# Performance work log

Measured on AMD Instinct MI355X. Metric: run time of the kernel, lower is better.

The kernel has to match this reference:

```python
import jax, jax.numpy as jnp
import numpy as np

L, D, H, FF = 6, 1024, 16, 4096
HD = D // H
EPS = 1e-5


def _ln(x, g, b):
    m = jnp.mean(x, axis=-1, keepdims=True)
    v = jnp.var(x, axis=-1, keepdims=True)
    return (x - m) * jax.lax.rsqrt(v + EPS) * g + b


def _heads(t, S, B):  # [S,B,D] -> [B*H,S,HD]
    return t.reshape(S, B * H, HD).swapaxes(0, 1)


def _attn(q, k, v, mask):
    # q,k,v: [B*H, Sq/Sk, HD]; q pre-scaled
    scores = jnp.einsum('bqd,bkd->bqk', q, k)
    if mask is not None:
        scores = scores + mask  # broadcast [1,Sq,Sk]
    p = jax.nn.softmax(scores, axis=-1)
    return jnp.einsum('bqk,bkd->bqd', p, v)


def _self_attn(x, w_qkv, b_qkv, w_out, b_out, mask):
    S, B, _ = x.shape
    qkv = x @ w_qkv.T + b_qkv  # [S,B,3D]
    q, k, v = jnp.split(qkv, 3, axis=-1)
    q = q * (HD ** -0.5)
    a = _attn(_heads(q, S, B), _heads(k, S, B), _heads(v, S, B), mask)
    a = a.swapaxes(0, 1).reshape(S, B, D)
    return a @ w_out.T + b_out


def _cross_attn(x, mem, w_q, b_q, w_kv, b_kv, w_out, b_out):
    S, B, _ = x.shape
    Sm = mem.shape[0]
    q = (x @ w_q.T + b_q) * (HD ** -0.5)
    kv = mem @ w_kv.T + b_kv  # [Sm,B,2D]
    k, v = jnp.split(kv, 2, axis=-1)
    a = _attn(_heads(q, S, B), _heads(k, Sm, B), _heads(v, Sm, B), None)
    a = a.swapaxes(0, 1).reshape(S, B, D)
    return a @ w_out.T + b_out


def _ffn(x, w1, b1, w2, b2):
    h = jax.nn.gelu(x @ w1.T + b1, approximate=False)
    return h @ w2.T + b2


def setup_inputs() -> dict:
    key = jax.random.key(0)
    ks = iter(jax.random.split(key, 64))
    def p(*shape, s=0.02):
        return (jax.random.normal(next(ks), shape, dtype=jnp.float32) * s)
    inp = {
        'src': jax.random.normal(next(ks), (512, 8, D), dtype=jnp.float32),
        'tgt': jax.random.normal(next(ks), (512, 8, D), dtype=jnp.float32),
        # encoder params (stacked over L layers)
        'enc_qkv_w': p(L, 3 * D, D), 'enc_qkv_b': p(L, 3 * D),
        'enc_out_w': p(L, D, D), 'enc_out_b': p(L, D),
        'enc_ln1_g': jnp.ones((L, D)), 'enc_ln1_b': jnp.zeros((L, D)),
        'enc_fc1_w': p(L, FF, D), 'enc_fc1_b': p(L, FF),
        'enc_fc2_w': p(L, D, FF), 'enc_fc2_b': p(L, D),
        'enc_ln2_g': jnp.ones((L, D)), 'enc_ln2_b': jnp.zeros((L, D)),
        'enc_norm_g': jnp.ones((D,)), 'enc_norm_b': jnp.zeros((D,)),
        # decoder params
        'dec_qkv_w': p(L, 3 * D, D), 'dec_qkv_b': p(L, 3 * D),
        'dec_sout_w': p(L, D, D), 'dec_sout_b': p(L, D),
        'dec_ln1_g': jnp.ones((L, D)), 'dec_ln1_b': jnp.zeros((L, D)),
        'dec_q_w': p(L, D, D), 'dec_q_b': p(L, D),
        'dec_kv_w': p(L, 2 * D, D), 'dec_kv_b': p(L, 2 * D),
        'dec_cout_w': p(L, D, D), 'dec_cout_b': p(L, D),
        'dec_ln2_g': jnp.ones((L, D)), 'dec_ln2_b': jnp.zeros((L, D)),
        'dec_fc1_w': p(L, FF, D), 'dec_fc1_b': p(L, FF),
        'dec_fc2_w': p(L, D, FF), 'dec_fc2_b': p(L, D),
        'dec_ln3_g': jnp.ones((L, D)), 'dec_ln3_b': jnp.zeros((L, D)),
        'dec_norm_g': jnp.ones((D,)), 'dec_norm_b': jnp.zeros((D,)),
    }
    return inp


def reference(src, tgt,
              enc_qkv_w, enc_qkv_b, enc_out_w, enc_out_b,
              enc_ln1_g, enc_ln1_b, enc_fc1_w, enc_fc1_b,
              enc_fc2_w, enc_fc2_b, enc_ln2_g, enc_ln2_b,
              enc_norm_g, enc_norm_b,
              dec_qkv_w, dec_qkv_b, dec_sout_w, dec_sout_b,
              dec_ln1_g, dec_ln1_b, dec_q_w, dec_q_b,
              dec_kv_w, dec_kv_b, dec_cout_w, dec_cout_b,
              dec_ln2_g, dec_ln2_b, dec_fc1_w, dec_fc1_b,
              dec_fc2_w, dec_fc2_b, dec_ln3_g, dec_ln3_b,
              dec_norm_g, dec_norm_b):
    St = tgt.shape[0]
    # causal additive mask [1,St,St]
    causal = jnp.where(jnp.tril(jnp.ones((St, St), dtype=bool)), 0.0, -jnp.inf)
    causal = causal[None].astype(src.dtype)

    # ---- encoder ----
    x = src
    for i in range(L):
        x = x + _self_attn(_ln(x, enc_ln1_g[i], enc_ln1_b[i]),
                           enc_qkv_w[i], enc_qkv_b[i], enc_out_w[i], enc_out_b[i], None)
        x = x + _ffn(_ln(x, enc_ln2_g[i], enc_ln2_b[i]),
                     enc_fc1_w[i], enc_fc1_b[i], enc_fc2_w[i], enc_fc2_b[i])
    memory = _ln(x, enc_norm_g, enc_norm_b)

    # ---- decoder ----
    y = tgt
    for i in range(L):
        y = y + _self_attn(_ln(y, dec_ln1_g[i], dec_ln1_b[i]),
                           dec_qkv_w[i], dec_qkv_b[i], dec_sout_w[i], dec_sout_b[i], causal)
        y = y + _cross_attn(_ln(y, dec_ln2_g[i], dec_ln2_b[i]), memory,
                            dec_q_w[i], dec_q_b[i], dec_kv_w[i], dec_kv_b[i],
                            dec_cout_w[i], dec_cout_b[i])
        y = y + _ffn(_ln(y, dec_ln3_g[i], dec_ln3_b[i]),
                     dec_fc1_w[i], dec_fc1_b[i], dec_fc2_w[i], dec_fc2_b[i])
    return _ln(y, dec_norm_g, dec_norm_b)
```

## Files before the change

kernel.cpp:

```cpp
#include <hip/hip_runtime.h>

typedef __attribute__((ext_vector_type(4))) float f32x4;
typedef __attribute__((ext_vector_type(8))) short short8;
typedef unsigned int u32;
typedef unsigned short u16;
typedef __attribute__((ext_vector_type(2))) u32 u32x2;
typedef __attribute__((ext_vector_type(4))) u32 u32x4;

#define DEV __device__ __forceinline__
#define GBAR __builtin_amdgcn_s_barrier()
#define SB0  __builtin_amdgcn_sched_barrier(0)

DEV u16 f2b(float f){
  u32 u = __builtin_bit_cast(u32, f);
  u32 r = u + 0x7fffu + ((u >> 16) & 1u);
  return (u16)(r >> 16);
}
DEV u32 pk2(float a, float b){ return (u32)f2b(a) | ((u32)f2b(b) << 16); }

DEV void gload16(const void* g, void* l){
  __builtin_amdgcn_global_load_lds((const __attribute__((address_space(1))) void*)g,
                                   (__attribute__((address_space(3))) void*)l, 16, 0, 0);
}
DEV u32 lds_addr(void* p){
  return (u32)(unsigned long long)(__attribute__((address_space(3))) char*)p;
}

__global__ __launch_bounds__(256) void cvt_k(const float* __restrict__ in,
                                             u16* __restrict__ out, int n8)
{
  int i = blockIdx.x*256 + threadIdx.x;
  const int stride = gridDim.x*256;
  for (; i < n8; i += stride){
    const float4 a = ((const float4*)in)[2*i];
    const float4 b = ((const float4*)in)[2*i+1];
    u32x4 r;
    r.x = pk2(a.x,a.y); r.y = pk2(a.z,a.w);
    r.z = pk2(b.x,b.y); r.w = pk2(b.z,b.w);
    ((u32x4*)out)[i] = r;
  }
}

template<int OUT_F32>
__global__ __launch_bounds__(256) void ln_k(const float* __restrict__ x,
    const float* __restrict__ gam, const float* __restrict__ bet,
    void* __restrict__ out)
{
  const int row = blockIdx.x, tid = threadIdx.x;
  const float4 v = ((const float4*)(x + row*1024))[tid];
  float s = (v.x + v.y) + (v.z + v.w);
  float q = (v.x*v.x + v.y*v.y) + (v.z*v.z + v.w*v.w);
  #pragma unroll
  for (int m = 1; m < 64; m <<= 1){ s += __shfl_xor(s, m); q += __shfl_xor(q, m); }
  __shared__ float ps[4], pq[4];
  if ((tid & 63) == 0){ ps[tid>>6] = s; pq[tid>>6] = q; }
  __syncthreads();
  s = (ps[0]+ps[1]) + (ps[2]+ps[3]);
  q = (pq[0]+pq[1]) + (pq[2]+pq[3]);
  const float mean = s * (1.f/1024.f);
  const float var  = q * (1.f/1024.f) - mean*mean;
  const float rstd = rsqrtf(var + 1e-5f);
  const float4 gg = ((const float4*)gam)[tid];
  const float4 bb = ((const float4*)bet)[tid];
  const float o0 = (v.x-mean)*rstd*gg.x + bb.x;
  const float o1 = (v.y-mean)*rstd*gg.y + bb.y;
  const float o2 = (v.z-mean)*rstd*gg.z + bb.z;
  const float o3 = (v.w-mean)*rstd*gg.w + bb.w;
  if (OUT_F32){
    float4 r; r.x=o0; r.y=o1; r.z=o2; r.w=o3;
    ((float4*)out)[row*256 + tid] = r;
  } else {
    u32x2 r; r.x = pk2(o0,o1); r.y = pk2(o2,o3);
    ((u32x2*)out)[row*256 + tid] = r;
  }
}

template<int DO_GELU, int DO_RES, int OUT_F32>
__global__ __launch_bounds__(256,2) void gemm_k(
    const u16* __restrict__ A, const u16* __restrict__ W,
    const float* __restrict__ bias, const float* __restrict__ res,
    void* __restrict__ Cout, int M, int N, int K)
{
  __shared__ char sA[16384];
  __shared__ char sB[16384];
  const int tid = threadIdx.x;
  const int lane = tid & 63, w = tid >> 6;
  const int wr = w >> 1, wc = w & 1;
  const int g = lane >> 4, c16 = lane & 15;

  const u32 nwg = gridDim.x * gridDim.y;
  u32 flat = blockIdx.x + gridDim.x * blockIdx.y;
  {
    const u32 q = nwg >> 3, r = nwg & 7;
    const u32 xcd = flat & 7, idx = flat >> 3;
    flat = (xcd < r ? xcd*(q+1) : r*(q+1) + (xcd-r)*q) + idx;
  }
  const int m0 = (int)(flat % gridDim.x) * 128;
  const int n0 = (int)(flat / gridDim.x) * 128;

  f32x4 acc[4][4];
  #pragma unroll
  for (int m = 0; m < 4; m++)
    #pragma unroll
    for (int n = 0; n < 4; n++) acc[m][n] = (f32x4){0.f,0.f,0.f,0.f};

  const int arow = tid >> 3, achk = tid & 7;
  const int acg = achk ^ (arow & 7);
  const u16* aSrc = A + (size_t)(m0 + arow)*K + acg*8;
  const u16* wSrc = W + (size_t)(n0 + arow)*K + acg*8;
  char* aDst = sA + w*1024;
  char* bDst = sB + w*1024;

  for (int kk = 0; kk < K; kk += 64){
    __syncthreads();
    #pragma unroll
    for (int i = 0; i < 4; i++){
      gload16(aSrc + (size_t)i*32*K + kk, aDst + i*4096);
      gload16(wSrc + (size_t)i*32*K + kk, bDst + i*4096);
    }
    __syncthreads();
    #pragma unroll
    for (int ks = 0; ks < 2; ks++){
      short8 af[4], bf[4];
      #pragma unroll
      for (int m = 0; m < 4; m++){
        const int row = wr*64 + m*16 + c16;
        af[m] = *(const short8*)(sA + row*128 + (((ks*4 + g) ^ (row & 7)) << 4));
      }
      #pragma unroll
      for (int n = 0; n < 4; n++){
        const int row = wc*64 + n*16 + c16;
        bf[n] = *(const short8*)(sB + row*128 + (((ks*4 + g) ^ (row & 7)) << 4));
      }
      #pragma unroll
      for (int m = 0; m < 4; m++)
        #pragma unroll
        for (int n = 0; n < 4; n++)
          acc[m][n] = __builtin_amdgcn_mfma_f32_16x16x32_bf16(af[m], bf[n], acc[m][n], 0,0,0);
    }
  }
  #pragma unroll
  for (int n = 0; n < 4; n++){
    const int col = n0 + wc*64 + n*16 + c16;
    const float bv = bias[col];
    #pragma unroll
    for (int m = 0; m < 4; m++){
      const int rbase = m0 + wr*64 + m*16 + g*4;
      #pragma unroll
      for (int r = 0; r < 4; r++){
        float v = acc[m][n][r] + bv;
        if (DO_GELU) v = 0.5f*v*(1.f + erff(v*0.70710678118654752f));
        if (DO_RES)  v += res[(size_t)(rbase + r)*N + col];
        if (OUT_F32) ((float*)Cout)[(size_t)(rbase + r)*N + col] = v;
        else         ((u16*)Cout)[(size_t)(rbase + r)*N + col] = f2b(v);
      }
    }
  }
}

template<int DO_GELU, int DO_RES, int OUT_F32>
__global__ __launch_bounds__(256,2) void gemm64_k(
    const u16* __restrict__ A, const u16* __restrict__ W,
    const float* __restrict__ bias, const float* __restrict__ res,
    void* __restrict__ Cout, int M, int N, int K)
{
  __shared__ char sA[8192];
  __shared__ char sB[8192];
  const int tid = threadIdx.x;
  const int lane = tid & 63, w = tid >> 6;
  const int wr = w >> 1, wc = w & 1;
  const int g = lane >> 4, c16 = lane & 15;

  const u32 nwg = gridDim.x * gridDim.y;
  u32 flat = blockIdx.x + gridDim.x * blockIdx.y;
  {
    const u32 q = nwg >> 3, r = nwg & 7;
    const u32 xcd = flat & 7, idx = flat >> 3;
    flat = (xcd < r ? xcd*(q+1) : r*(q+1) + (xcd-r)*q) + idx;
  }
  const int m0 = (int)(flat % gridDim.x) * 64;
  const int n0 = (int)(flat / gridDim.x) * 64;

  f32x4 acc[2][2];
  #pragma unroll
  for (int m = 0; m < 2; m++)
    #pragma unroll
    for (int n = 0; n < 2; n++) acc[m][n] = (f32x4){0.f,0.f,0.f,0.f};

  const int arow = tid >> 3, achk = tid & 7;
  const int acg = achk ^ (arow & 7);
  const u16* aSrc = A + (size_t)(m0 + arow)*K + acg*8;
  const u16* wSrc = W + (size_t)(n0 + arow)*K + acg*8;
  char* aDst = sA + w*1024;
  char* bDst = sB + w*1024;

  for (int kk = 0; kk < K; kk += 64){
    __syncthreads();
    #pragma unroll
    for (int i = 0; i < 2; i++){
      gload16(aSrc + (size_t)i*32*K + kk, aDst + i*4096);
      gload16(wSrc + (size_t)i*32*K + kk, bDst + i*4096);
    }
    __syncthreads();
    #pragma unroll
    for (int ks = 0; ks < 2; ks++){
      short8 af[2], bf[2];
      #pragma unroll
      for (int m = 0; m < 2; m++){
        const int row = wr*32 + m*16 + c16;
        af[m] = *(const short8*)(sA + row*128 + (((ks*4 + g) ^ (row & 7)) << 4));
      }
      #pragma unroll
      for (int n = 0; n < 2; n++){
        const int row = wc*32 + n*16 + c16;
        bf[n] = *(const short8*)(sB + row*128 + (((ks*4 + g) ^ (row & 7)) << 4));
      }
      #pragma unroll
      for (int m = 0; m < 2; m++)
        #pragma unroll
        for (int n = 0; n < 2; n++)
          acc[m][n] = __builtin_amdgcn_mfma_f32_16x16x32_bf16(af[m], bf[n], acc[m][n], 0,0,0);
    }
  }
  #pragma unroll
  for (int n = 0; n < 2; n++){
    const int col = n0 + wc*32 + n*16 + c16;
    const float bv = bias[col];
    #pragma unroll
    for (int m = 0; m < 2; m++){
      const int rbase = m0 + wr*32 + m*16 + g*4;
      #pragma unroll
      for (int r = 0; r < 4; r++){
        float v = acc[m][n][r] + bv;
        if (DO_GELU) v = 0.5f*v*(1.f + erff(v*0.70710678118654752f));
        if (DO_RES)  v += res[(size_t)(rbase + r)*N + col];
        if (OUT_F32) ((float*)Cout)[(size_t)(rbase + r)*N + col] = v;
        else         ((u16*)Cout)[(size_t)(rbase + r)*N + col] = f2b(v);
      }
    }
  }
}

template<int CAUSAL>
__global__ __launch_bounds__(256,2) void attn_k(
    const u16* __restrict__ Qb, int qB, int qS,
    const u16* __restrict__ Kb, int kB, int kS,
    const u16* __restrict__ Vb, int vB, int vS,
    u16* __restrict__ Ob, int oB, int oS, float scale)
{
  __shared__ char smem[16384];
  const int tid = threadIdx.x;
  const int lane = tid & 63, w = tid >> 6;
  const int g = lane >> 4, c16 = lane & 15;
  const int qt = blockIdx.x, bh = blockIdx.y;
  const int b = bh >> 4, h = bh & 15;
  const u16* Q  = Qb + b*qB + h*64;
  const u16* Kp = Kb + b*kB + h*64;
  const u16* Vp = Vb + b*vB + h*64;
  u16*       Op = Ob + b*oB + h*64;

  const int qrow = qt*64 + w*16 + c16;
  const short8 bq0 = *(const short8*)(Q + qrow*qS + g*8);
  const short8 bq1 = *(const short8*)(Q + qrow*qS + 32 + g*8);

  f32x4 o[4];
  #pragma unroll
  for (int d = 0; d < 4; d++) o[d] = (f32x4){0.f,0.f,0.f,0.f};
  float mrun = -__builtin_inff(), lrun = 0.f;

  const int srow = tid >> 3, schk = tid & 7;
  const u16* kSrc = Kp + srow*kS + (schk ^ (srow & 7))*8;
  const u16* vSrc = Vp + srow*vS + schk*8;
  const u32 vtr0 = lds_addr(smem) + 8192 + (8*g + (c16 >> 2))*128 + (c16 & 3)*8;

  auto STAGE = [&](int p, int j0){
    gload16(kSrc + (size_t)j0*kS, smem + p*4096 + w*1024);
    gload16(vSrc + (size_t)j0*vS, smem + 8192 + p*4096 + w*1024);
  };
  auto COMPUTE = [&](int p, int j0){
    char* Ks = smem + p*4096;
    f32x4 st[2];
    #pragma unroll
    for (int t = 0; t < 2; t++){
      const int row = t*16 + c16;
      const int rx = row & 7;
      const short8 ka0 = *(const short8*)(Ks + row*128 + ((g ^ rx) << 4));
      const short8 ka1 = *(const short8*)(Ks + row*128 + (((4 + g) ^ rx) << 4));
      f32x4 z = (f32x4){0.f,0.f,0.f,0.f};
      z = __builtin_amdgcn_mfma_f32_16x16x32_bf16(ka0, bq0, z, 0,0,0);
      z = __builtin_amdgcn_mfma_f32_16x16x32_bf16(ka1, bq1, z, 0,0,0);
      st[t] = z;
    }
    float mloc = -__builtin_inff();
    #pragma unroll
    for (int t = 0; t < 2; t++)
      #pragma unroll
      for (int r = 0; r < 4; r++){
        float sv = st[t][r]*scale;
        if (CAUSAL){ if (j0 + t*16 + g*4 + r > qrow) sv = -__builtin_inff(); }
        st[t][r] = sv;
        mloc = fmaxf(mloc, sv);
      }
    mloc = fmaxf(mloc, __shfl_xor(mloc, 16));
    mloc = fmaxf(mloc, __shfl_xor(mloc, 32));
    const float mnew = fmaxf(mrun, mloc);
    const float corr = __expf(mrun - mnew);
    float psum = 0.f;
    u32 pk00, pk01, pk10, pk11;
    {
      float p0 = __expf(st[0][0]-mnew), p1 = __expf(st[0][1]-mnew);
      float p2 = __expf(st[0][2]-mnew), p3 = __expf(st[0][3]-mnew);
      psum += (p0+p1) + (p2+p3);
      pk00 = pk2(p0,p1); pk01 = pk2(p2,p3);
      p0 = __expf(st[1][0]-mnew); p1 = __expf(st[1][1]-mnew);
      p2 = __expf(st[1][2]-mnew); p3 = __expf(st[1][3]-mnew);
      psum += (p0+p1) + (p2+p3);
      pk10 = pk2(p0,p1); pk11 = pk2(p2,p3);
    }
    psum += __shfl_xor(psum, 16);
    psum += __shfl_xor(psum, 32);
    lrun = lrun*corr + psum;
    mrun = mnew;
    #pragma unroll
    for (int d = 0; d < 4; d++){
      o[d][0]*=corr; o[d][1]*=corr; o[d][2]*=corr; o[d][3]*=corr;
    }
    const int sl0 = c16 | (((g << 1)     & 3) << 4);
    const int sl1 = c16 | ((((g << 1)+1) & 3) << 4);
    const u32 a00 = (u32)__shfl((int)pk00, sl0), a01 = (u32)__shfl((int)pk01, sl0);
    const u32 a02 = (u32)__shfl((int)pk00, sl1), a03 = (u32)__shfl((int)pk01, sl1);
    const u32 a10 = (u32)__shfl((int)pk10, sl0), a11 = (u32)__shfl((int)pk11, sl0);
    const u32 a12 = (u32)__shfl((int)pk10, sl1), a13 = (u32)__shfl((int)pk11, sl1);
    const bool hi = g >= 2;
    union { short8 s; u32 u[4]; } pb;
    pb.u[0] = hi ? a10 : a00;
    pb.u[1] = hi ? a11 : a01;
    pb.u[2] = hi ? a12 : a02;
    pb.u[3] = hi ? a13 : a03;

    const u32 vtr = vtr0 + p*4096;
    u32x2 t00,t01,t10,t11,t20,t21,t30,t31;
    asm volatile("ds_read_b64_tr_b16 %0, %1 offset:0"   : "=v"(t00) : "v"(vtr));
    asm volatile("ds_read_b64_tr_b16 %0, %1 offset:512" : "=v"(t01) : "v"(vtr));
    asm volatile("ds_read_b64_tr_b16 %0, %1 offset:32"  : "=v"(t10) : "v"(vtr));
    asm volatile("ds_read_b64_tr_b16 %0, %1 offset:544" : "=v"(t11) : "v"(vtr));
    asm volatile("ds_read_b64_tr_b16 %0, %1 offset:64"  : "=v"(t20) : "v"(vtr));
    asm volatile("ds_read_b64_tr_b16 %0, %1 offset:576" : "=v"(t21) : "v"(vtr));
    asm volatile("ds_read_b64_tr_b16 %0, %1 offset:96"  : "=v"(t30) : "v"(vtr));
    asm volatile("ds_read_b64_tr_b16 %0, %1 offset:608" : "=v"(t31) : "v"(vtr));
    asm volatile("s_waitcnt lgkmcnt(0)" ::: "memory");
    __builtin_amdgcn_sched_barrier(0);
    union { short8 s; u32x2 d[2]; } v0u, v1u, v2u, v3u;
    v0u.d[0]=t00; v0u.d[1]=t01;
    v1u.d[0]=t10; v1u.d[1]=t11;
    v2u.d[0]=t20; v2u.d[1]=t21;
    v3u.d[0]=t30; v3u.d[1]=t31;
    o[0] = __builtin_amdgcn_mfma_f32_16x16x32_bf16(v0u.s, pb.s, o[0], 0,0,0);
    o[1] = __builtin_amdgcn_mfma_f32_16x16x32_bf16(v1u.s, pb.s, o[1], 0,0,0);
    o[2] = __builtin_amdgcn_mfma_f32_16x16x32_bf16(v2u.s, pb.s, o[2], 0,0,0);
    o[3] = __builtin_amdgcn_mfma_f32_16x16x32_bf16(v3u.s, pb.s, o[3], 0,0,0);
  };

  const int nCh = CAUSAL ? (2*qt + 2) : 16;
  STAGE(0, 0);
  for (int jc = 0; jc < nCh - 1; ++jc){
    STAGE((jc+1) & 1, (jc+1)*32);
    asm volatile("s_waitcnt vmcnt(2)" ::: "memory");
    GBAR; SB0;
    COMPUTE(jc & 1, jc*32);
    SB0; GBAR;
  }
  asm volatile("s_waitcnt vmcnt(0)" ::: "memory");
  GBAR; SB0;
  COMPUTE((nCh-1) & 1, (nCh-1)*32);
  SB0; GBAR;

  const float inv = 1.f / lrun;
  char* Olds = smem;
  #pragma unroll
  for (int dd = 0; dd < 4; dd++){
    u32x2 val;
    val.x = pk2(o[dd][0]*inv, o[dd][1]*inv);
    val.y = pk2(o[dd][2]*inv, o[dd][3]*inv);
    const int row = w*16 + c16;
    const int off = 32*dd + 8*g;
    const int chunk = off >> 4, rem = off & 15;
    *(u32x2*)(Olds + row*128 + ((chunk ^ (row & 7)) << 4) + rem) = val;
  }
  __syncthreads();
  const int orow = tid >> 2, oc = tid & 3;
  #pragma unroll
  for (int i = 0; i < 2; i++){
    const int ch = oc*2 + i;
    const u32x4 vv = *(const u32x4*)(Olds + orow*128 + ((ch ^ (orow & 7)) << 4));
    *(u32x4*)(Op + (qt*64 + orow)*oS + ch*8) = vv;
  }
}

static inline int cvt_grid(int n8){ int g = (n8 + 255) / 256; return g > 2048 ? 2048 : g; }

extern "C" void kernel_launch(void* const* d_in, const int* in_sizes, int n_in,
                              void* d_out, int out_size, void* d_ws, size_t ws_size,
                              hipStream_t stream)
{
  (void)in_sizes; (void)n_in; (void)out_size; (void)ws_size;
  const float* src      = (const float*)d_in[0];
  const float* tgt      = (const float*)d_in[1];
  const float* e_qkv_w  = (const float*)d_in[2];
  const float* e_qkv_b  = (const float*)d_in[3];
  const float* e_out_w  = (const float*)d_in[4];
  const float* e_out_b  = (const float*)d_in[5];
  const float* e_ln1_g  = (const float*)d_in[6];
  const float* e_ln1_b  = (const float*)d_in[7];
  const float* e_fc1_w  = (const float*)d_in[8];
  const float* e_fc1_b  = (const float*)d_in[9];
  const float* e_fc2_w  = (const float*)d_in[10];
  const float* e_fc2_b  = (const float*)d_in[11];
  const float* e_ln2_g  = (const float*)d_in[12];
  const float* e_ln2_b  = (const float*)d_in[13];
  const float* e_nrm_g  = (const float*)d_in[14];
  const float* e_nrm_b  = (const float*)d_in[15];
  const float* dc_qkv_w = (const float*)d_in[16];
  const float* dc_qkv_b = (const float*)d_in[17];
  const float* dc_sout_w= (const float*)d_in[18];
  const float* dc_sout_b= (const float*)d_in[19];
  const float* dc_ln1_g = (const float*)d_in[20];
  const float* dc_ln1_b = (const float*)d_in[21];
  const float* dc_q_w   = (const float*)d_in[22];
  const float* dc_q_b   = (const float*)d_in[23];
  const float* dc_kv_w  = (const float*)d_in[24];
  const float* dc_kv_b  = (const float*)d_in[25];
  const float* dc_cout_w= (const float*)d_in[26];
  const float* dc_cout_b= (const float*)d_in[27];
  const float* dc_ln2_g = (const float*)d_in[28];
  const float* dc_ln2_b = (const float*)d_in[29];
  const float* dc_fc1_w = (const float*)d_in[30];
  const float* dc_fc1_b = (const float*)d_in[31];
  const float* dc_fc2_w = (const float*)d_in[32];
  const float* dc_fc2_b = (const float*)d_in[33];
  const float* dc_ln3_g = (const float*)d_in[34];
  const float* dc_ln3_b = (const float*)d_in[35];
  const float* dc_nrm_g = (const float*)d_in[36];
  const float* dc_nrm_b = (const float*)d_in[37];

  char* ws = (char*)d_ws;
  u16*  ln_out = (u16*)(ws);
  u16*  attn_o = (u16*)(ws + (8u<<20));
  u16*  membuf = (u16*)(ws + (16u<<20));
  float* xres  = (float*)(ws + (24u<<20));
  u16*  region = (u16*)(ws + (40u<<20));
  u16*  qkv   = region;
  u16*  hbuf  = region;
  u16*  qbuf  = region;
  u16*  kvbuf = region + (4u<<20);

  const dim3 blk(256);
  const int M = 4096;

  u16* wb = (u16*)(ws + (72u<<20));
  size_t woff = 0;
  auto CV = [&](const float* wsrc, size_t n)->u16* {
    u16* p = wb + woff; woff += n;
    cvt_k<<<cvt_grid((int)(n >> 3)), blk, 0, stream>>>(wsrc, p, (int)(n >> 3));
    return p;
  };
  u16* Weqkv = CV(e_qkv_w,  6ull*3072*1024);
  u16* Weout = CV(e_out_w,  6ull*1024*1024);
  u16* Wefc1 = CV(e_fc1_w,  6ull*4096*1024);
  u16* Wefc2 = CV(e_fc2_w,  6ull*4096*1024);
  u16* Wdqkv = CV(dc_qkv_w, 6ull*3072*1024);
  u16* Wdsout= CV(dc_sout_w,6ull*1024*1024);
  u16* Wdq   = CV(dc_q_w,   6ull*1024*1024);
  u16* Wdkv  = CV(dc_kv_w,  6ull*2048*1024);
  u16* Wdcout= CV(dc_cout_w,6ull*1024*1024);
  u16* Wdfc1 = CV(dc_fc1_w, 6ull*4096*1024);
  u16* Wdfc2 = CV(dc_fc2_w, 6ull*4096*1024);

  for (int i = 0; i < 6; i++){
    const float* xin = i ? xres : src;
    ln_k<0><<<4096, blk, 0, stream>>>(xin, e_ln1_g + i*1024, e_ln1_b + i*1024, ln_out);
    gemm_k<0,0,0><<<dim3(32, 24), blk, 0, stream>>>(ln_out,
        Weqkv + (size_t)i*3145728, e_qkv_b + i*3072, nullptr, qkv, M, 3072, 1024);
    attn_k<0><<<dim3(8,128), blk, 0, stream>>>(qkv, 3072, 24576,
        qkv+1024, 3072, 24576, qkv+2048, 3072, 24576, attn_o, 1024, 8192, 0.125f);
    gemm64_k<0,1,1><<<dim3(64, 16), blk, 0, stream>>>(attn_o,
        Weout + (size_t)i*1048576, e_out_b + i*1024, xin, xres, M, 1024, 1024);
    ln_k<0><<<4096, blk, 0, stream>>>(xres, e_ln2_g + i*1024, e_ln2_b + i*1024, ln_out);
    gemm_k<1,0,0><<<dim3(32, 32), blk, 0, stream>>>(ln_out,
        Wefc1 + (size_t)i*4194304, e_fc1_b + i*4096, nullptr, hbuf, M, 4096, 1024);
    gemm64_k<0,1,1><<<dim3(64, 16), blk, 0, stream>>>(hbuf,
        Wefc2 + (size_t)i*4194304, e_fc2_b + i*1024, xres, xres, M, 1024, 4096);
  }
  ln_k<0><<<4096, blk, 0, stream>>>(xres, e_nrm_g, e_nrm_b, membuf);

  for (int i = 0; i < 6; i++){
    const float* yin = i ? xres : tgt;
    ln_k<0><<<4096, blk, 0, stream>>>(yin, dc_ln1_g + i*1024, dc_ln1_b + i*1024, ln_out);
    gemm_k<0,0,0><<<dim3(32, 24), blk, 0, stream>>>(ln_out,
        Wdqkv + (size_t)i*3145728, dc_qkv_b + i*3072, nullptr, qkv, M, 3072, 1024);
    attn_k<1><<<dim3(8,128), blk, 0, stream>>>(qkv, 3072, 24576,
        qkv+1024, 3072, 24576, qkv+2048, 3072, 24576, attn_o, 1024, 8192, 0.125f);
    gemm64_k<0,1,1><<<dim3(64, 16), blk, 0, stream>>>(attn_o,
        Wdsout + (size_t)i*1048576, dc_sout_b + i*1024, yin, xres, M, 1024, 1024);
    ln_k<0><<<4096, blk, 0, stream>>>(xres, dc_ln2_g + i*1024, dc_ln2_b + i*1024, ln_out);
    gemm64_k<0,0,0><<<dim3(64, 16), blk, 0, stream>>>(ln_out,
        Wdq + (size_t)i*1048576, dc_q_b + i*1024, nullptr, qbuf, M, 1024, 1024);
    gemm64_k<0,0,0><<<dim3(64, 32), blk, 0, stream>>>(membuf,
        Wdkv + (size_t)i*2097152, dc_kv_b + i*2048, nullptr, kvbuf, M, 2048, 1024);
    attn_k<0><<<dim3(8,128), blk, 0, stream>>>(qbuf, 1024, 8192,
        kvbuf, 2048, 16384, kvbuf+1024, 2048, 16384, attn_o, 1024, 8192, 0.125f);
    gemm64_k<0,1,1><<<dim3(64, 16), blk, 0, stream>>>(attn_o,
        Wdcout + (size_t)i*1048576, dc_cout_b + i*1024, xres, xres, M, 1024, 1024);
    ln_k<0><<<4096, blk, 0, stream>>>(xres, dc_ln3_g + i*1024, dc_ln3_b + i*1024, ln_out);
    gemm_k<1,0,0><<<dim3(32, 32), blk, 0, stream>>>(ln_out,
        Wdfc1 + (size_t)i*4194304, dc_fc1_b + i*4096, nullptr, hbuf, M, 4096, 1024);
    gemm64_k<0,1,1><<<dim3(64, 16), blk, 0, stream>>>(hbuf,
        Wdfc2 + (size_t)i*4194304, dc_fc2_b + i*1024, xres, xres, M, 1024, 4096);
  }
  ln_k<1><<<4096, blk, 0, stream>>>(xres, dc_nrm_g, dc_nrm_b, d_out);
}
```

Baseline: 3.719 ms.

## Add 256x256-tile 8-wave GEMM for QKV and FC1 projections

Adds a new 512-thread GEMM kernel with 256x256 output tiles, 128KB double-buffered LDS and interleaved global-to-LDS staging across four MFMA phases per K step. It replaces the older 128-tile gemm_k for the QKV and FC1 (with GELU) projections, to raise operand reuse and cut global/LDS traffic per FLOP. The grids shrink to 192 and 256 workgroups, which can leave CUs idle or underfilled on a 256-CU device. The epilogue writes bf16 with scalar strided stores. The barrier macro also switches from the builtin to inline-asm s_barrier with a memory clobber.

```diff
diff --git a/kernel.cpp b/kernel.cpp
--- a/kernel.cpp
+++ b/kernel.cpp
@@ -8,8 +8,8 @@
 typedef __attribute__((ext_vector_type(4))) u32 u32x4;
 
 #define DEV __device__ __forceinline__
-#define GBAR __builtin_amdgcn_s_barrier()
 #define SB0  __builtin_amdgcn_sched_barrier(0)
+#define HBAR asm volatile("s_barrier" ::: "memory")
 
 DEV u16 f2b(float f){
   u32 u = __builtin_bit_cast(u32, f);
@@ -72,6 +72,151 @@
   } else {
     u32x2 r; r.x = pk2(o0,o1); r.y = pk2(o2,o3);
     ((u32x2*)out)[row*256 + tid] = r;
+  }
+}
+
+template<int DO_GELU>
+__global__ __launch_bounds__(512,2) void gemm256_k(
+    const u16* __restrict__ A, const u16* __restrict__ W,
+    const float* __restrict__ bias, u16* __restrict__ Cout,
+    int M, int N, int K)
+{
+  __shared__ char lds[131072];
+  const int tid = threadIdx.x;
+  const int lane = tid & 63, wid = tid >> 6;
+  const int wr = wid >> 2, wc = wid & 3;
+  const int g = lane >> 4, c16 = lane & 15;
+
+  const u32 nwg = gridDim.x * gridDim.y;
+  u32 flat = blockIdx.x + gridDim.x * blockIdx.y;
+  {
+    const u32 q = nwg >> 3, r = nwg & 7;
+    const u32 xcd = flat & 7, idx = flat >> 3;
+    flat = (xcd < r ? xcd*(q+1) : r*(q+1) + (xcd-r)*q) + idx;
+  }
+  const int m0 = (int)(flat % gridDim.x) * 256;
+  const int n0 = (int)(flat / gridDim.x) * 256;
+
+  f32x4 acc[8][4];
+  #pragma unroll
+  for (int m = 0; m < 8; m++)
+    #pragma unroll
+    for (int n = 0; n < 4; n++) acc[m][n] = (f32x4){0.f,0.f,0.f,0.f};
+
+  const int srow = tid >> 3, schk = tid & 7;
+  const int scg = schk ^ (srow & 7);
+  const u16* aS = A + (size_t)(m0 + srow)*K + scg*8;
+  const u16* wS = W + (size_t)(n0 + srow)*K + scg*8;
+
+  auto SG = [&](const u16* base, int regionOff, int sb, int half, int i, int kk){
+    gload16(base + (size_t)(half*128 + i*64)*K + kk,
+            lds + sb*65536 + regionOff + half*16384 + i*8192 + tid*16);
+  };
+  short8 af[4][2], bf[4][2];
+  auto LDA4 = [&](char* bufA, int mbase){
+    #pragma unroll
+    for (int i = 0; i < 4; i++){
+      const int r = (mbase + i)*16 + c16;
+      const int rx = r & 7;
+      af[i][0] = *(const short8*)(bufA + r*128 + ((g ^ rx) << 4));
+      af[i][1] = *(const short8*)(bufA + r*128 + (((4 + g) ^ rx) << 4));
+    }
+  };
+  auto LDB2 = [&](char* bufB, int nbase){
+    #pragma unroll
+    for (int i = 0; i < 2; i++){
+      const int r = (wc & 1)*64 + (nbase + i)*16 + c16;
+      const int rx = r & 7;
+      bf[nbase+i][0] = *(const short8*)(bufB + r*128 + ((g ^ rx) << 4));
+      bf[nbase+i][1] = *(const short8*)(bufB + r*128 + (((4 + g) ^ rx) << 4));
+    }
+  };
+
+  const int NT = K >> 6;
+  SG(wS, 32768, 0, 0, 0, 0); SG(wS, 32768, 0, 0, 1, 0);
+  SG(wS, 32768, 0, 1, 0, 0); SG(wS, 32768, 0, 1, 1, 0);
+  SG(aS, 0,     0, 0, 0, 0); SG(aS, 0,     0, 0, 1, 0);
+  SG(aS, 0,     0, 1, 0, 0); SG(aS, 0,     0, 1, 1, 0);
+  asm volatile("s_waitcnt vmcnt(1)" ::: "memory");
+  HBAR;
+
+  for (int t = 0; t < NT; ++t){
+    const int b = t & 1, sb = b ^ 1;
+    const int skk = (t+1) << 6;
+    const bool st = (t+1 < NT);
+    char* bufA = lds + b*65536 + wr*16384;
+    char* bufB = lds + b*65536 + 32768 + (wc >> 1)*16384;
+
+    LDA4(bufA, 0); LDB2(bufB, 0);
+    if (st){ SG(wS, 32768, sb, 0, 0, skk); SG(wS, 32768, sb, 0, 1, skk); }
+    HBAR;
+    asm volatile("s_waitcnt lgkmcnt(0)" ::: "memory"); SB0;
+    __builtin_amdgcn_s_setprio(1);
+    #pragma unroll
+    for (int ks = 0; ks < 2; ks++)
+      #pragma unroll
+      for (int i = 0; i < 4; i++)
+        #pragma unroll
+        for (int j = 0; j < 2; j++)
+          acc[i][j] = __builtin_amdgcn_mfma_f32_16x16x32_bf16(af[i][ks], bf[j][ks], acc[i][j], 0,0,0);
+    __builtin_amdgcn_s_setprio(0);
+    LDB2(bufB, 2);
+    if (st){ SG(wS, 32768, sb, 1, 0, skk); SG(wS, 32768, sb, 1, 1, skk); }
+    HBAR;
+    asm volatile("s_waitcnt lgkmcnt(0)" ::: "memory"); SB0;
+    __builtin_amdgcn_s_setprio(1);
+    #pragma unroll
+    for (int ks = 0; ks < 2; ks++)
+      #pragma unroll
+      for (int i = 0; i < 4; i++)
+        #pragma unroll
+        for (int j = 2; j < 4; j++)
+          acc[i][j] = __builtin_amdgcn_mfma_f32_16x16x32_bf16(af[i][ks], bf[j][ks], acc[i][j], 0,0,0);
+    __builtin_amdgcn_s_setprio(0);
+    if (st) asm volatile("s_waitcnt vmcnt(4)" ::: "memory");
+    else    asm volatile("s_waitcnt vmcnt(0)" ::: "memory");
+    HBAR;
+    LDA4(bufA, 4);
+    if (st){ SG(aS, 0, sb, 0, 0, skk); SG(aS, 0, sb, 0, 1, skk); }
+    asm volatile("s_waitcnt lgkmcnt(0)" ::: "memory"); SB0;
+    __builtin_amdgcn_s_setprio(1);
+    #pragma unroll
+    for (int ks = 0; ks < 2; ks++)
+      #pragma unroll
+      for (int i = 0; i < 4; i++)
+        #pragma unroll
+        for (int j = 0; j < 2; j++)
+          acc[4+i][j] = __builtin_amdgcn_mfma_f32_16x16x32_bf16(af[i][ks], bf[j][ks], acc[4+i][j], 0,0,0);
+    __builtin_amdgcn_s_setprio(0);
+    if (st){ SG(aS, 0, sb, 1, 0, skk); SG(aS, 0, sb, 1, 1, skk); }
+    HBAR;
+    __builtin_amdgcn_s_setprio(1);
+    #pragma unroll
+    for (int ks = 0; ks < 2; ks++)
+      #pragma unroll
+      for (int i = 0; i < 4; i++)
+        #pragma unroll
+        for (int j = 2; j < 4; j++)
+          acc[4+i][j] = __builtin_amdgcn_mfma_f32_16x16x32_bf16(af[i][ks], bf[j][ks], acc[4+i][j], 0,0,0);
+    __builtin_amdgcn_s_setprio(0);
+    if (st) asm volatile("s_waitcnt vmcnt(1)" ::: "memory");
+    HBAR;
+  }
+
+  #pragma unroll
+  for (int n = 0; n < 4; n++){
+    const int col = n0 + wc*64 + n*16 + c16;
+    const float bv = bias[col];
+    #pragma unroll
+    for (int m = 0; m < 8; m++){
+      const int rbase = m0 + wr*128 + m*16 + g*4;
+      #pragma unroll
+      for (int r = 0; r < 4; r++){
+        float v = acc[m][n][r] + bv;
+        if (DO_GELU) v = 0.5f*v*(1.f + erff(v*0.70710678118654752f));
+        Cout[(size_t)(rbase + r)*N + col] = f2b(v);
+      }
+    }
   }
 }
 
@@ -366,14 +511,14 @@
   for (int jc = 0; jc < nCh - 1; ++jc){
     STAGE((jc+1) & 1, (jc+1)*32);
     asm volatile("s_waitcnt vmcnt(2)" ::: "memory");
-    GBAR; SB0;
+    HBAR; SB0;
     COMPUTE(jc & 1, jc*32);
-    SB0; GBAR;
+    SB0; HBAR;
   }
   asm volatile("s_waitcnt vmcnt(0)" ::: "memory");
-  GBAR; SB0;
+  HBAR; SB0;
   COMPUTE((nCh-1) & 1, (nCh-1)*32);
-  SB0; GBAR;
+  SB0; HBAR;
 
   const float inv = 1.f / lrun;
   char* Olds = smem;
@@ -455,6 +600,7 @@
   u16*  kvbuf = region + (4u<<20);
 
   const dim3 blk(256);
+  const dim3 blk512(512);
   const int M = 4096;
 
   u16* wb = (u16*)(ws + (72u<<20));
@@ -479,15 +625,15 @@
   for (int i = 0; i < 6; i++){
     const float* xin = i ? xres : src;
     ln_k<0><<<4096, blk, 0, stream>>>(xin, e_ln1_g + i*1024, e_ln1_b + i*1024, ln_out);
-    gemm_k<0,0,0><<<dim3(32, 24), blk, 0, stream>>>(ln_out,
-        Weqkv + (size_t)i*3145728, e_qkv_b + i*3072, nullptr, qkv, M, 3072, 1024);
+    gemm256_k<0><<<dim3(16, 12), blk512, 0, stream>>>(ln_out,
+        Weqkv + (size_t)i*3145728, e_qkv_b + i*3072, qkv, M, 3072, 1024);
     attn_k<0><<<dim3(8,128), blk, 0, stream>>>(qkv, 3072, 24576,
         qkv+1024, 3072, 24576, qkv+2048, 3072, 24576, attn_o, 1024, 8192, 0.125f);
     gemm64_k<0,1,1><<<dim3(64, 16), blk, 0, stream>>>(attn_o,
         Weout + (size_t)i*1048576, e_out_b + i*1024, xin, xres, M, 1024, 1024);
     ln_k<0><<<4096, blk, 0, stream>>>(xres, e_ln2_g + i*1024, e_ln2_b + i*1024, ln_out);
-    gemm_k<1,0,0><<<dim3(32, 32), blk, 0, stream>>>(ln_out,
-        Wefc1 + (size_t)i*4194304, e_fc1_b + i*4096, nullptr, hbuf, M, 4096, 1024);
+    gemm256_k<1><<<dim3(16, 16), blk512, 0, stream>>>(ln_out,
+        Wefc1 + (size_t)i*4194304, e_fc1_b + i*4096, hbuf, M, 4096, 1024);
     gemm64_k<0,1,1><<<dim3(64, 16), blk, 0, stream>>>(hbuf,
         Wefc2 + (size_t)i*4194304, e_fc2_b + i*1024, xres, xres, M, 1024, 4096);
   }
@@ -496,8 +642,8 @@
   for (int i = 0; i < 6; i++){
     const float* yin = i ? xres : tgt;
     ln_k<0><<<4096, blk, 0, stream>>>(yin, dc_ln1_g + i*1024, dc_ln1_b + i*1024, ln_out);
-    gemm_k<0,0,0><<<dim3(32, 24), blk, 0, stream>>>(ln_out,
-        Wdqkv + (size_t)i*3145728, dc_qkv_b + i*3072, nullptr, qkv, M, 3072, 1024);
+    gemm256_k<0><<<dim3(16, 12), blk512, 0, stream>>>(ln_out,
+        Wdqkv + (size_t)i*3145728, dc_qkv_b + i*3072, qkv, M, 3072, 1024);
     attn_k<1><<<dim3(8,128), blk, 0, stream>>>(qkv, 3072, 24576,
         qkv+1024, 3072, 24576, qkv+2048, 3072, 24576, attn_o, 1024, 8192, 0.125f);
     gemm64_k<0,1,1><<<dim3(64, 16), blk, 0, stream>>>(attn_o,
@@ -512,8 +658,8 @@
     gemm64_k<0,1,1><<<dim3(64, 16), blk, 0, stream>>>(attn_o,
         Wdcout + (size_t)i*1048576, dc_cout_b + i*1024, xres, xres, M, 1024, 1024);
     ln_k<0><<<4096, blk, 0, stream>>>(xres, dc_ln3_g + i*1024, dc_ln3_b + i*1024, ln_out);
-    gemm_k<1,0,0><<<dim3(32, 32), blk, 0, stream>>>(ln_out,
-        Wdfc1 + (size_t)i*4194304, dc_fc1_b + i*4096, nullptr, hbuf, M, 4096, 1024);
+    gemm256_k<1><<<dim3(16, 16), blk512, 0, stream>>>(ln_out,
+        Wdfc1 + (size_t)i*4194304, dc_fc1_b + i*4096, hbuf, M, 4096, 1024);
     gemm64_k<0,1,1><<<dim3(64, 16), blk, 0, stream>>>(hbuf,
         Wdfc2 + (size_t)i*4194304, dc_fc2_b + i*1024, xres, xres, M, 1024, 4096);
   }
```

After: 3.615 ms. 2.8% less time.
